# Optimization experiments

Measured on AMD Instinct MI355X. Metric: run time of the kernel, lower is better.

The kernel has to match this reference:

```python
import jax, jax.numpy as jnp
import numpy as np

N = 80000
E = 1280000
EPS = 1e-5

def _lrelu(x):
    return jax.nn.leaky_relu(x, 0.01)

def _bn(h):
    # training-mode BatchNorm1d with batch size 1: stats over the node dim; affine is identity at init
    return (h - h.mean(0)) / jnp.sqrt(h.var(0) + EPS)

def _ln(h, g, b):
    m = h.mean(-1, keepdims=True)
    v = h.var(-1, keepdims=True)
    return (h - m) / jnp.sqrt(v + EPS) * g + b

def _gcn(h, w, b, src, dst, n):
    # PyG GCNConv: add self loops, symmetric deg^-1/2 normalization, aggregate at target
    hw = h @ w.T
    loop = jnp.arange(n, dtype=src.dtype)
    s = jnp.concatenate([src, loop])
    d = jnp.concatenate([dst, loop])
    deg = jax.ops.segment_sum(jnp.ones(d.shape, hw.dtype), d, num_segments=n)
    dinv = jnp.where(deg > 0, 1.0 / jnp.sqrt(deg), 0.0)
    msg = hw[s] * (dinv[s] * dinv[d])[:, None]  # [E+N, C]
    return jax.ops.segment_sum(msg, d, num_segments=n) + b

def _tnet(x, c1w, c1b, c2w, c2b, c3w, c3b, f1w, f1b, f2w, f2b, f3w, f3b):
    h = jax.nn.relu(x @ c1w.T + c1b)          # [N,64]  (source skips bn1)
    h = jax.nn.relu(_bn(h @ c2w.T + c2b))     # [N,128]
    h = jax.nn.relu(_bn(h @ c3w.T + c3b))     # [N,1024]
    g = h.max(0)                              # global max pool -> [1024]
    g = jax.nn.relu(g @ f1w.T + f1b)
    g = jax.nn.relu(g @ f2w.T + f2b)
    iden = jnp.array([1.0, 0.0, 0.0, 0.0, 1.0, 0.0, 0.0, 0.0, 1.0], x.dtype)
    g = g @ f3w.T + f3b + iden
    return g.reshape(3, 3)

def _forward(edge_index, x, tnet_c1_w, tnet_c1_b, tnet_c2_w, tnet_c2_b, tnet_c3_w, tnet_c3_b, tnet_fc1_w, tnet_fc1_b, tnet_fc2_w, tnet_fc2_b, tnet_fc3_w, tnet_fc3_b, conv1_w, conv1_b, g1_li_w, g1_li_b, g1_gcn_w, g1_gcn_b, g1_ln_g, g1_ln_b, conv2_w, conv2_b, g2_li_w, g2_li_b, g2_gcn_w, g2_gcn_b, g2_ln_g, g2_ln_b, conv3_w, conv3_b, out_w, out_b):
    src, dst = edge_index[0], edge_index[1]
    n = x.shape[0]
    T = _tnet(x, tnet_c1_w, tnet_c1_b, tnet_c2_w, tnet_c2_b, tnet_c3_w, tnet_c3_b, tnet_fc1_w, tnet_fc1_b, tnet_fc2_w, tnet_fc2_b, tnet_fc3_w, tnet_fc3_b)
    h0 = x @ T                                  # [N,3] spatial transform
    xg = _lrelu(h0 @ conv1_w.T + conv1_b)       # [N,64] (conv1d k=1 == per-node linear)
    # Gcn_Attention 1
    nf = _lrelu(xg @ g1_li_w.T + g1_li_b)
    nf2 = _lrelu(_gcn(nf, g1_gcn_w, g1_gcn_b, src, dst, n))
    h = _ln(jnp.concatenate([nf, nf2], 1), g1_ln_g, g1_ln_b)   # [N,128]
    h = _lrelu(h @ conv2_w.T + conv2_b)
    # Gcn_Attention 2
    nf = _lrelu(h @ g2_li_w.T + g2_li_b)
    nf2 = _lrelu(_gcn(nf, g2_gcn_w, g2_gcn_b, src, dst, n))
    h = _ln(jnp.concatenate([nf, nf2], 1), g2_ln_g, g2_ln_b)   # [N,256]
    h = jnp.concatenate([h, xg], 1)                            # [N,320]
    h = _lrelu(h @ conv3_w.T + conv3_b)                        # [N,256]
    pooled = h.mean(0)                                         # global mean pool (single graph)
    feat = jnp.concatenate([jnp.broadcast_to(pooled, (n, pooled.shape[0])), xg], 1)  # [N,320]
    return feat @ out_w.T + out_b                              # [N,4]

def setup_inputs():
    ki = iter(jax.random.split(jax.random.key(0), 32))
    def W(shape):
        return jax.random.normal(next(ki), shape, jnp.float32) * (1.0 / float(np.sqrt(shape[-1])))
    z = lambda n: jnp.zeros((n,), jnp.float32)
    o = lambda n: jnp.ones((n,), jnp.float32)
    inp = {}
    inp['x'] = jax.random.normal(next(ki), (N, 3), jnp.float32)
    inp['edge_index'] = jax.random.randint(next(ki), (2, E), 0, N, dtype=jnp.int32)
    inp['tnet_c1_w'] = W((64, 3)); inp['tnet_c1_b'] = z(64)
    inp['tnet_c2_w'] = W((128, 64)); inp['tnet_c2_b'] = z(128)
    inp['tnet_c3_w'] = W((1024, 128)); inp['tnet_c3_b'] = z(1024)
    inp['tnet_fc1_w'] = W((512, 1024)); inp['tnet_fc1_b'] = z(512)
    inp['tnet_fc2_w'] = W((256, 512)); inp['tnet_fc2_b'] = z(256)
    inp['tnet_fc3_w'] = W((9, 256)); inp['tnet_fc3_b'] = z(9)
    inp['conv1_w'] = W((64, 3)); inp['conv1_b'] = z(64)
    inp['g1_li_w'] = W((64, 64)); inp['g1_li_b'] = z(64)
    inp['g1_gcn_w'] = W((64, 64)); inp['g1_gcn_b'] = z(64)
    inp['g1_ln_g'] = o(128); inp['g1_ln_b'] = z(128)
    inp['conv2_w'] = W((128, 128)); inp['conv2_b'] = z(128)
    inp['g2_li_w'] = W((128, 128)); inp['g2_li_b'] = z(128)
    inp['g2_gcn_w'] = W((128, 128)); inp['g2_gcn_b'] = z(128)
    inp['g2_ln_g'] = o(256); inp['g2_ln_b'] = z(256)
    inp['conv3_w'] = W((256, 320)); inp['conv3_b'] = z(256)
    inp['out_w'] = W((4, 320)); inp['out_b'] = z(4)
    return inp

def reference(x, edge_index, tnet_c1_w, tnet_c1_b, tnet_c2_w, tnet_c2_b, tnet_c3_w, tnet_c3_b, tnet_fc1_w, tnet_fc1_b, tnet_fc2_w, tnet_fc2_b, tnet_fc3_w, tnet_fc3_b, conv1_w, conv1_b, g1_li_w, g1_li_b, g1_gcn_w, g1_gcn_b, g1_ln_g, g1_ln_b, conv2_w, conv2_b, g2_li_w, g2_li_b, g2_gcn_w, g2_gcn_b, g2_ln_g, g2_ln_b, conv3_w, conv3_b, out_w, out_b):
    return _forward(edge_index, x, tnet_c1_w, tnet_c1_b, tnet_c2_w, tnet_c2_b, tnet_c3_w, tnet_c3_b, tnet_fc1_w, tnet_fc1_b, tnet_fc2_w, tnet_fc2_b, tnet_fc3_w, tnet_fc3_b, conv1_w, conv1_b, g1_li_w, g1_li_b, g1_gcn_w, g1_gcn_b, g1_ln_g, g1_ln_b, conv2_w, conv2_b, g2_li_w, g2_li_b, g2_gcn_w, g2_gcn_b, g2_ln_g, g2_ln_b, conv3_w, conv3_b, out_w, out_b)
```

## Files before the change

kernel.cpp:

```cpp
#include <hip/hip_runtime.h>
#include <cstddef>

#define EPSV 1e-5f

typedef __attribute__((ext_vector_type(8))) short frag8;
typedef __attribute__((ext_vector_type(4))) float f32x4;

__device__ __forceinline__ float lrelu01(float v) { return v > 0.f ? v : 0.01f * v; }
__device__ __forceinline__ void atomAddF(float* p, float v) { unsafeAtomicAdd(p, v); }
__device__ __forceinline__ unsigned fkey(float f) {
    unsigned u = __float_as_uint(f);
    return (u & 0x80000000u) ? ~u : (u | 0x80000000u);
}
__device__ __forceinline__ unsigned short f2b(float f) {
    unsigned u = __float_as_uint(f);
    unsigned r = u + 0x7fffu + ((u >> 16) & 1u);
    return (unsigned short)(r >> 16);
}
__device__ __forceinline__ float b2f(unsigned short h) {
    return __uint_as_float(((unsigned)h) << 16);
}
__device__ __forceinline__ float blo(unsigned u) { return __uint_as_float(u << 16); }
__device__ __forceinline__ float bhi(unsigned u) { return __uint_as_float(u & 0xffff0000u); }

static inline unsigned cdivu(unsigned a, unsigned b) { return (a + b - 1) / b; }


__device__ void degrank_body(int bid, const int* __restrict__ dst, int* __restrict__ deg,
                             int* __restrict__ rank, int E) {
    int e = bid * 256 + threadIdx.x;
    if (e < E) rank[e] = atomicAdd(&deg[dst[e]], 1);
}

__device__ void scan_local_body(int bid, const int* __restrict__ deg, int* __restrict__ startv,
                                int* __restrict__ bsum, float* __restrict__ dinv, int n) {
    __shared__ int t0[256];
    int tid = threadIdx.x;
    int i = bid * 256 + tid;
    int v = (i < n) ? deg[i] : 0;
    if (i < n) dinv[i] = rsqrtf((float)(v + 1));
    t0[tid] = v;
    __syncthreads();
    for (int o = 1; o < 256; o <<= 1) {
        int add = (tid >= o) ? t0[tid - o] : 0;
        __syncthreads();
        t0[tid] += add;
        __syncthreads();
    }
    if (i < n) startv[i] = t0[tid] - v;
    if (tid == 255) bsum[bid] = t0[255];
}

__device__ void scan_bsum_body(int* __restrict__ bsum, int nb) {
    __shared__ int t0[512];
    __shared__ int t1[512];
    int tid = threadIdx.x;
    int v0 = (tid < nb) ? bsum[tid] : 0;
    int v1 = (tid + 256 < nb) ? bsum[tid + 256] : 0;
    t0[tid] = v0; t0[tid + 256] = v1;
    __syncthreads();
    int* a = t0; int* b = t1;
    for (int o = 1; o < 512; o <<= 1) {
        b[tid]       = a[tid]       + ((tid >= o)       ? a[tid - o]       : 0);
        b[tid + 256] = a[tid + 256] + ((tid + 256 >= o) ? a[tid + 256 - o] : 0);
        __syncthreads();
        int* t = a; a = b; b = t;
    }
    if (tid < nb) bsum[tid] = a[tid] - v0;
    if (tid + 256 < nb) bsum[tid + 256] = a[tid + 256] - v1;
}

__device__ void scan_add_body(int bid, int* __restrict__ startv, const int* __restrict__ bsum, int n) {
    int i = bid * 256 + threadIdx.x;
    if (i < n) startv[i] += bsum[bid];
}

__device__ void fill_body(int bid, const int* __restrict__ src, const int* __restrict__ dst,
                          const int* __restrict__ rank, const int* __restrict__ startv,
                          int* __restrict__ csr, int E) {
    int e = bid * 256 + threadIdx.x;
    if (e < E) csr[startv[dst[e]] + rank[e]] = src[e];
}


__device__ void wconv_body(int bid, const float* __restrict__ s0, const float* __restrict__ s1,
                           const float* __restrict__ s2, const float* __restrict__ s3,
                           const float* __restrict__ s4, const float* __restrict__ s5,
                           const float* __restrict__ s6, const float* __restrict__ s7,
                           unsigned short* __restrict__ dst) {
    int t = bid * 256 + threadIdx.x;
    if (t >= 278528) return;
    const float* srcs[8] = {s0, s1, s2, s3, s4, s5, s6, s7};
    const int off[9] = {0, 8192, 139264, 143360, 147456, 163840, 180224, 196608, 278528};
    int seg = 0;
    while (t >= off[seg + 1]) ++seg;
    unsigned short v = f2b(srcs[seg][t - off[seg]]);
    if (seg == 1) {
        int li = t - 8192;
        int rch = li >> 7, k = li & 127;
        int cb = rch >> 7, r = rch & 127;
        int flat = ((r >> 4) * 4 + (k >> 5)) * 64 + ((k >> 3) & 3) * 16 + (r & 15);
        dst[8192 + cb * 16384 + flat * 8 + (k & 7)] = v;
    } else {
        dst[t] = v;
    }
}

__device__ void h1_body(int bid, const float* __restrict__ x, const float* __restrict__ w,
                        const float* __restrict__ b, unsigned short* __restrict__ h1, int n) {
    int node = bid * 256 + threadIdx.x;
    if (node >= n) return;
    float x0 = x[node * 3], x1 = x[node * 3 + 1], x2 = x[node * 3 + 2];
    unsigned short* o = h1 + (size_t)node * 64;
#pragma unroll
    for (int cp = 0; cp < 8; ++cp) {
        unsigned short tmp[8];
#pragma unroll
        for (int t = 0; t < 8; ++t) {
            int c = cp * 8 + t;
            float v = x0 * w[c * 3] + x1 * w[c * 3 + 1] + x2 * w[c * 3 + 2] + b[c];
            tmp[t] = f2b(fmaxf(v, 0.f));
        }
        *(float4*)(o + cp * 8) = *(float4*)tmp;
    }
}

__device__ void prebn_body(int bid, const float* __restrict__ z, const float* __restrict__ sum2,
                           const float* __restrict__ ss2, unsigned short* __restrict__ a3f,
                           int n16, float invn) {
    int t = bid * 256 + threadIdx.x;
    if (t >= n16) return;
    int row = t >> 4, cp = t & 15;
    int c = cp * 8;
    const float* src = z + (size_t)row * 128 + c;
    float4 v0 = *(const float4*)src;
    float4 v1 = *(const float4*)(src + 4);
    float vv[8] = {v0.x, v0.y, v0.z, v0.w, v1.x, v1.y, v1.z, v1.w};
    unsigned short o[8];
#pragma unroll
    for (int i = 0; i < 8; ++i) {
        float m = sum2[c + i] * invn;
        float var = ss2[c + i] * invn - m * m;
        o[i] = f2b(fmaxf((vv[i] - m) * rsqrtf(var + EPSV), 0.f));
    }
    int tile = row >> 7, r = row & 127;
    int flat = ((r >> 4) * 4 + (cp >> 2)) * 64 + (cp & 3) * 16 + (r & 15);
    *(float4*)(a3f + (size_t)tile * 16384 + flat * 8) = *(float4*)o;
}

__device__ void fc1_body(int bid, const float* __restrict__ sum3, const float* __restrict__ ss3,
                         const unsigned* __restrict__ maxk,
                         const float* __restrict__ f1w, const float* __restrict__ f1b,
                         float* __restrict__ a1, float invn) {
    __shared__ float g[1024];
    int tid = threadIdx.x;
    for (int c = tid; c < 1024; c += 256) {
        float m = sum3[c] * invn;
        float var = ss3[c] * invn - m * m;
        unsigned k = maxk[c];
        unsigned u = (k & 0x80000000u) ? (k & 0x7FFFFFFFu) : ~k;
        g[c] = fmaxf((__uint_as_float(u) - m) * rsqrtf(var + EPSV), 0.f);
    }
    __syncthreads();
    int row = bid * 64 + (tid >> 2);
    int part = tid & 3;
    const float* w = f1w + (size_t)row * 1024 + part * 256;
    const float* gg = g + part * 256;
    float s = 0.f;
#pragma unroll 4
    for (int k = 0; k < 256; k += 4) {
        float4 wv = *(const float4*)(w + k);
        s = fmaf(wv.x, gg[k], s);
        s = fmaf(wv.y, gg[k + 1], s);
        s = fmaf(wv.z, gg[k + 2], s);
        s = fmaf(wv.w, gg[k + 3], s);
    }
    s += __shfl_xor(s, 1); s += __shfl_xor(s, 2);
    if (part == 0) a1[row] = fmaxf(s + f1b[row], 0.f);
}

enum { MF_BIAS = 1, MF_LRELU = 2, MF_DINV = 4, MF_STOREF = 8, MF_STOREB = 16,
       MF_STATS = 32, MF_COLSUM = 64 };

template <int BN, int MODE>
__device__ void mgemm_body(int bx, int by,
                           const unsigned short* __restrict__ A, int lda, int K,
                           const unsigned short* __restrict__ W,
                           const float* __restrict__ bias,
                           float* __restrict__ OutF, unsigned short* __restrict__ OutB, int ldo,
                           const float* __restrict__ dinv,
                           float* __restrict__ sum_o, float* __restrict__ ss_o,
                           unsigned* __restrict__ maxk_o) {
    constexpr int BM = 128;
    constexpr int LDT = 40;
    __shared__ unsigned short As[BM * LDT];
    __shared__ unsigned short Ws[BN * LDT];
    __shared__ float redS[2 * 128];
    __shared__ unsigned redM[128];

    const int tid = threadIdx.x;
    const int wid = tid >> 6, lane = tid & 63;
    const int quad = lane >> 4, lrow = lane & 15;
    const int bn0 = bx * BM;
    const int bc0 = by * BN;

    constexpr int NI = (BN == 128) ? 4 : 2;
    constexpr int NJ = 4;
    const int wm = (BN == 128) ? (wid & 1) * 64 : wid * 32;
    const int wn = (BN == 128) ? (wid >> 1) * 64 : 0;

    if (MODE & (MF_STATS | MF_COLSUM)) {
        for (int c = tid; c < BN; c += 256) {
            redS[c] = 0.f; redS[128 + c] = 0.f; redM[c] = 0u;
        }
    }

    f32x4 acc[NI][NJ] = {};

    for (int k0 = 0; k0 < K; k0 += 32) {
#pragma unroll
        for (int h = 0; h < 2; ++h) {
            int ch = tid + h * 256;
            int row = ch >> 2, cp = ch & 3;
            const unsigned short* src = A + (size_t)(bn0 + row) * lda + k0 + cp * 8;
            *(float4*)&As[row * LDT + cp * 8] = *(const float4*)src;
        }
#pragma unroll
        for (int h = 0; h < BN / 64; ++h) {
            int ch = tid + h * 256;
            int row = ch >> 2, cp = ch & 3;
            const unsigned short* src = W + (size_t)(bc0 + row) * K + k0 + cp * 8;
            *(float4*)&Ws[row * LDT + cp * 8] = *(const float4*)src;
        }
        __syncthreads();
        frag8 af[NI], bf[NJ];
#pragma unroll
        for (int i = 0; i < NI; ++i)
            af[i] = *(const frag8*)&As[(wm + i * 16 + lrow) * LDT + quad * 8];
#pragma unroll
        for (int j = 0; j < NJ; ++j)
            bf[j] = *(const frag8*)&Ws[(wn + j * 16 + lrow) * LDT + quad * 8];
#pragma unroll
        for (int i = 0; i < NI; ++i)
#pragma unroll
            for (int j = 0; j < NJ; ++j)
                acc[i][j] = __builtin_amdgcn_mfma_f32_16x16x32_bf16(af[i], bf[j], acc[i][j], 0, 0, 0);
        __syncthreads();
    }

#pragma unroll
    for (int j = 0; j < NJ; ++j) {
        const int col = bc0 + wn + j * 16 + lrow;
        float bv = (MODE & MF_BIAS) ? bias[col] : 0.f;
        float s = 0.f, q = 0.f, m = -3.4e38f;
#pragma unroll
        for (int i = 0; i < NI; ++i) {
            const int rowb = bn0 + wm + i * 16 + quad * 4;
#pragma unroll
            for (int r = 0; r < 4; ++r) {
                float t = acc[i][j][r] + bv;
                if (MODE & MF_LRELU) t = lrelu01(t);
                if (MODE & MF_DINV) t *= dinv[rowb + r];
                if (MODE & MF_STOREF) OutF[(size_t)(rowb + r) * ldo + col] = t;
                if (MODE & MF_STOREB) OutB[(size_t)(rowb + r) * ldo + col] = f2b(t);
                s += t; q += t * t; m = fmaxf(m, t);
            }
        }
        if (MODE & (MF_STATS | MF_COLSUM)) {
            s += __shfl_xor(s, 16); s += __shfl_xor(s, 32);
            if (MODE & MF_STATS) {
                q += __shfl_xor(q, 16); q += __shfl_xor(q, 32);
                m = fmaxf(m, __shfl_xor(m, 16)); m = fmaxf(m, __shfl_xor(m, 32));
            }
            if (quad == 0) {
                int lc = wn + j * 16 + lrow;
                atomicAdd(&redS[lc], s);
                if (MODE & MF_STATS) {
                    atomicAdd(&redS[128 + lc], q);
                    atomicMax(&redM[lc], fkey(m));
                }
            }
        }
    }
    if (MODE & (MF_STATS | MF_COLSUM)) {
        __syncthreads();
        for (int c = tid; c < BN; c += 256) {
            atomAddF(&sum_o[bc0 + c], redS[c]);
            if (MODE & MF_STATS) {
                atomAddF(&ss_o[bc0 + c], redS[128 + c]);
                atomicMax(&maxk_o[bc0 + c], redM[c]);
            }
        }
    }
}

template <int BN, int MODE, int SWAP>
__launch_bounds__(256)
__global__ void k_mgemm(const unsigned short* __restrict__ A, int lda, int K,
                        const unsigned short* __restrict__ W,
                        const float* __restrict__ bias,
                        float* __restrict__ OutF, unsigned short* __restrict__ OutB, int ldo,
                        const float* __restrict__ dinv,
                        float* __restrict__ sum_o, float* __restrict__ ss_o,
                        unsigned* __restrict__ maxk_o) {
    int bx = SWAP ? blockIdx.y : blockIdx.x;
    int by = SWAP ? blockIdx.x : blockIdx.y;
    mgemm_body<BN, MODE>(bx, by, A, lda, K, W, bias, OutF, OutB, ldo, dinv, sum_o, ss_o, maxk_o);
}

__device__ void z3_body(int bid,
                        const unsigned short* __restrict__ AF,
                        const unsigned short* __restrict__ WF,
                        const float* __restrict__ bias,
                        float* __restrict__ sum_o, float* __restrict__ ss_o,
                        unsigned* __restrict__ maxk_o, int ntiles) {
    const int tid = threadIdx.x;
    const int wid = tid >> 6, lane = tid & 63;
    const int quad = lane >> 4, lrow = lane & 15;

    int w = (bid & 7) * ntiles + (bid >> 3);
    const int tile = w >> 3;
    const int cb = w & 7;
    const unsigned short* At = AF + (size_t)tile * 16384;
    const unsigned short* Wt = WF + (size_t)cb * 16384;

    const int ar = (wid & 1) * 4;
    const int wc = (wid >> 1) * 4;
    f32x4 acc[4][4] = {};
#pragma unroll
    for (int kc = 0; kc < 4; ++kc) {
        frag8 af[4], bf[4];
#pragma unroll
        for (int i = 0; i < 4; ++i)
            af[i] = *(const frag8*)&At[(((ar + i) * 4 + kc) * 64 + lane) * 8];
#pragma unroll
        for (int j = 0; j < 4; ++j)
            bf[j] = *(const frag8*)&Wt[(((wc + j) * 4 + kc) * 64 + lane) * 8];
#pragma unroll
        for (int i = 0; i < 4; ++i)
#pragma unroll
            for (int j = 0; j < 4; ++j)
                acc[i][j] = __builtin_amdgcn_mfma_f32_16x16x32_bf16(af[i], bf[j], acc[i][j], 0, 0, 0);
    }

#pragma unroll
    for (int j = 0; j < 4; ++j) {
        int c = cb * 128 + (wc + j) * 16 + lrow;
        float bv = bias[c];
        float s = 0.f, q = 0.f, m = -3.4e38f;
#pragma unroll
        for (int i = 0; i < 4; ++i)
#pragma unroll
            for (int r = 0; r < 4; ++r) {
                float t = acc[i][j][r] + bv;
                s += t; q += t * t; m = fmaxf(m, t);
            }
        s += __shfl_xor(s, 16); s += __shfl_xor(s, 32);
        q += __shfl_xor(q, 16); q += __shfl_xor(q, 32);
        m = fmaxf(m, __shfl_xor(m, 16)); m = fmaxf(m, __shfl_xor(m, 32));
        if (quad == 0) {
            atomAddF(&sum_o[c], s);
            atomAddF(&ss_o[c], q);
            atomicMax(&maxk_o[c], fkey(m));
        }
    }
}


__launch_bounds__(256)
__global__ void FK1(const int* __restrict__ dst, int* __restrict__ deg, int* __restrict__ rank,
                    int E, int EB,
                    const float* s0, const float* s1, const float* s2, const float* s3,
                    const float* s4, const float* s5, const float* s6, const float* s7,
                    unsigned short* __restrict__ WB, int WCB,
                    const float* __restrict__ x, const float* __restrict__ c1w,
                    const float* __restrict__ c1b, unsigned short* __restrict__ B1, int n) {
    int b = blockIdx.x;
    if (b < EB) { degrank_body(b, dst, deg, rank, E); return; }
    b -= EB;
    if (b < WCB) { wconv_body(b, s0, s1, s2, s3, s4, s5, s6, s7, WB); return; }
    b -= WCB;
    h1_body(b, x, c1w, c1b, B1, n);
}

__launch_bounds__(256)
__global__ void FK2(const unsigned short* __restrict__ A, int lda, int K,
                    const unsigned short* __restrict__ W, const float* __restrict__ bias,
                    float* __restrict__ OutF, int ldo,
                    float* __restrict__ sum_o, float* __restrict__ ss_o,
                    unsigned* __restrict__ maxk_o, int GXz,
                    const int* __restrict__ deg, int* __restrict__ startv,
                    int* __restrict__ bsum, float* __restrict__ dinvv, int n) {
    if ((int)blockIdx.x < GXz)
        mgemm_body<128, (MF_BIAS | MF_STOREF | MF_STATS)>(
            blockIdx.x, 0, A, lda, K, W, bias, OutF, nullptr, ldo, nullptr, sum_o, ss_o, maxk_o);
    else
        scan_local_body(blockIdx.x - GXz, deg, startv, bsum, dinvv, n);
}

__launch_bounds__(256)
__global__ void FK3(const float* __restrict__ z, const float* __restrict__ sum2,
                    const float* __restrict__ ss2, unsigned short* __restrict__ a3f,
                    int n16, float invn, int PB, int* __restrict__ bsum, int nb) {
    if ((int)blockIdx.x < PB) prebn_body(blockIdx.x, z, sum2, ss2, a3f, n16, invn);
    else scan_bsum_body(bsum, nb);
}

__launch_bounds__(256)
__global__ void FK4(const unsigned short* __restrict__ AF, const unsigned short* __restrict__ WF,
                    const float* __restrict__ bias,
                    float* __restrict__ sum_o, float* __restrict__ ss_o,
                    unsigned* __restrict__ maxk_o, int ntiles, int NZ,
                    int* __restrict__ startv, const int* __restrict__ bsum, int n) {
    if ((int)blockIdx.x < NZ) z3_body(blockIdx.x, AF, WF, bias, sum_o, ss_o, maxk_o, ntiles);
    else scan_add_body(blockIdx.x - NZ, startv, bsum, n);
}

__launch_bounds__(256)
__global__ void FK5(const int* __restrict__ src, const int* __restrict__ dst,
                    const int* __restrict__ rank, const int* __restrict__ startv,
                    int* __restrict__ csr, int E,
                    const float* __restrict__ sum3, const float* __restrict__ ss3,
                    const unsigned* __restrict__ maxk,
                    const float* __restrict__ f1w, const float* __restrict__ f1b,
                    float* __restrict__ a1, float invn) {
    int b = blockIdx.x;
    if (b < 8) { fc1_body(b, sum3, ss3, maxk, f1w, f1b, a1, invn); return; }
    fill_body(b - 8, src, dst, rank, startv, csr, E);
}

__launch_bounds__(256)
__global__ void k_fc2(const float* __restrict__ a1, const float* __restrict__ f2w,
                      const float* __restrict__ f2bias, float* __restrict__ a2) {
    __shared__ float a1s[512];
    int tid = threadIdx.x;
    a1s[tid] = a1[tid];
    a1s[tid + 256] = a1[tid + 256];
    __syncthreads();
    int row = blockIdx.x * 32 + (tid >> 3);
    int part = tid & 7;
    const float* w = f2w + (size_t)row * 512 + part * 64;
    const float* aa = a1s + part * 64;
    float s = 0.f;
#pragma unroll 4
    for (int k = 0; k < 64; k += 4) {
        float4 wv = *(const float4*)(w + k);
        s = fmaf(wv.x, aa[k], s);
        s = fmaf(wv.y, aa[k + 1], s);
        s = fmaf(wv.z, aa[k + 2], s);
        s = fmaf(wv.w, aa[k + 3], s);
    }
    s += __shfl_xor(s, 1); s += __shfl_xor(s, 2); s += __shfl_xor(s, 4);
    if (part == 0) a2[row] = fmaxf(s + f2bias[row], 0.f);
}

template <int CH>
__launch_bounds__(256)
__global__ void k_gln(const int* __restrict__ startv, const int* __restrict__ degv,
                      const int* __restrict__ csr, const unsigned short* __restrict__ q,
                      const unsigned short* __restrict__ nf, const float* __restrict__ dinv,
                      const float* __restrict__ gcn_b, const float* __restrict__ lng,
                      const float* __restrict__ lnb, unsigned short* __restrict__ outp,
                      int ldo, int n) {
    constexpr int GRP = (CH == 64) ? 8 : 4;
    constexpr int PL  = 64 / GRP;
    constexpr int TT  = 16 / GRP;
    constexpr int CPL = CH / PL;
    const int wv = threadIdx.x >> 6, lane = threadIdx.x & 63;
    const int g = lane / PL, p = lane & (PL - 1);
    int node = blockIdx.x * 4 + wv;
    if (node >= n) return;

    const unsigned short* qp = q + (size_t)p * CPL;

    float acc[CPL];
    {
        uint4 v = *(const uint4*)(qp + (size_t)node * CH);
        unsigned sv[4] = {v.x, v.y, v.z, v.w};
        if (g == 0) {
#pragma unroll
            for (int d = 0; d < 4; ++d) { acc[2 * d] = blo(sv[d]); acc[2 * d + 1] = bhi(sv[d]); }
        } else {
#pragma unroll
            for (int k = 0; k < CPL; ++k) acc[k] = 0.f;
        }
    }

    int s0 = startv[node], cnt = degv[node];
    const int* cs = csr + s0;
    int sidx[TT];
#pragma unroll
    for (int t = 0; t < TT; ++t) { int j = t * GRP + g; sidx[t] = (j < cnt) ? cs[j] : n; }
    for (int j0 = 0; j0 < cnt; j0 += 16) {
        uint4 buf[TT];
#pragma unroll
        for (int t = 0; t < TT; ++t)
            buf[t] = *(const uint4*)(qp + (size_t)(unsigned)sidx[t] * CH);
#pragma unroll
        for (int t = 0; t < TT; ++t) {
            int j = j0 + 16 + t * GRP + g;
            sidx[t] = (j < cnt) ? cs[j] : n;
        }
#pragma unroll
        for (int t = 0; t < TT; ++t) {
            unsigned bw[4] = {buf[t].x, buf[t].y, buf[t].z, buf[t].w};
#pragma unroll
            for (int d = 0; d < 4; ++d) {
                acc[2 * d] += blo(bw[d]);
                acc[2 * d + 1] += bhi(bw[d]);
            }
        }
    }

#pragma unroll
    for (int k = 0; k < CPL; ++k) {
#pragma unroll
        for (int off = PL; off < 64; off <<= 1) acc[k] += __shfl_xor(acc[k], off);
    }

    float di = dinv[node];
    float nv[CPL], bv[CPL];
    {
        uint4 v = *(const uint4*)(nf + (size_t)node * CH + p * CPL);
        unsigned sv[4] = {v.x, v.y, v.z, v.w};
#pragma unroll
        for (int d = 0; d < 4; ++d) { nv[2 * d] = blo(sv[d]); nv[2 * d + 1] = bhi(sv[d]); }
    }
    const float* gb = gcn_b + p * CPL;
#pragma unroll
    for (int k = 0; k < CPL; ++k) bv[k] = lrelu01(di * acc[k] + gb[k]);

    float s = 0.f, ss = 0.f;
#pragma unroll
    for (int k = 0; k < CPL; ++k) { s += nv[k] + bv[k]; ss += nv[k] * nv[k] + bv[k] * bv[k]; }
#pragma unroll
    for (int off = 32; off > 0; off >>= 1) { s += __shfl_xor(s, off); ss += __shfl_xor(ss, off); }
    const float inv = 1.f / (float)(GRP * 2 * CH);
    float mu = s * inv;
    float var = ss * inv - mu * mu;
    float rsg = rsqrtf(var + EPSV);

    unsigned short* orow = outp + (size_t)node * ldo;
    if (g == 0) {
        unsigned short tmp[CPL];
        const float* lg = lng + p * CPL; const float* lb = lnb + p * CPL;
#pragma unroll
        for (int k = 0; k < CPL; ++k) tmp[k] = f2b((nv[k] - mu) * rsg * lg[k] + lb[k]);
        *(uint4*)(orow + p * CPL) = *(uint4*)tmp;
    } else if (g == 1) {
        unsigned short tmp[CPL];
        const float* lg = lng + CH + p * CPL; const float* lb = lnb + CH + p * CPL;
#pragma unroll
        for (int k = 0; k < CPL; ++k) tmp[k] = f2b((bv[k] - mu) * rsg * lg[k] + lb[k]);
        *(uint4*)(orow + CH + p * CPL) = *(uint4*)tmp;
    }
}


__launch_bounds__(256)
__global__ void k_xg2(const float* __restrict__ x, const float* __restrict__ a2,
                      const float* __restrict__ f3w, const float* __restrict__ f3b,
                      const float* __restrict__ w, const float* __restrict__ b,
                      unsigned short* __restrict__ xg, int n) {
    __shared__ float a2s[256];
    __shared__ float T9s[9];
    int tid = threadIdx.x;
    a2s[tid] = a2[tid];
    __syncthreads();
    if (tid < 144) {
        int r = tid >> 4, kk = (tid & 15) * 16;
        const float* wr = f3w + r * 256 + kk;
        const float* ar = a2s + kk;
        float s = 0.f;
#pragma unroll
        for (int k = 0; k < 16; ++k) s = fmaf(wr[k], ar[k], s);
        s += __shfl_xor(s, 1); s += __shfl_xor(s, 2);
        s += __shfl_xor(s, 4); s += __shfl_xor(s, 8);
        if ((tid & 15) == 0) {
            s += f3b[r];
            if (r == 0 || r == 4 || r == 8) s += 1.f;
            T9s[r] = s;
        }
    }
    __syncthreads();
    int node = blockIdx.x * 256 + tid;
    if (node >= n) return;
    float x0 = x[node * 3], x1 = x[node * 3 + 1], x2 = x[node * 3 + 2];
    float h0 = x0 * T9s[0] + x1 * T9s[3] + x2 * T9s[6];
    float h1 = x0 * T9s[1] + x1 * T9s[4] + x2 * T9s[7];
    float h2 = x0 * T9s[2] + x1 * T9s[5] + x2 * T9s[8];
    unsigned short* o = xg + (size_t)node * 320;
#pragma unroll
    for (int cp = 0; cp < 8; ++cp) {
        unsigned short tmp[8];
#pragma unroll
        for (int t = 0; t < 8; ++t) {
            int c = cp * 8 + t;
            float v = h0 * w[c * 3] + h1 * w[c * 3 + 1] + h2 * w[c * 3 + 2] + b[c];
            tmp[t] = f2b(lrelu01(v));
        }
        *(float4*)(o + cp * 8) = *(float4*)tmp;
    }
}

template <int BN>
__launch_bounds__(256)
__global__ void k_ligc(const unsigned short* __restrict__ A, int lda, int K,
                       const unsigned short* __restrict__ Wli, const float* __restrict__ bli,
                       const unsigned short* __restrict__ Wgc, const float* __restrict__ dinv,
                       unsigned short* __restrict__ NF, int ldnf,
                       unsigned short* __restrict__ Q, int ldq) {
    constexpr int BM = 128;
    constexpr int LDT = 40;
    constexpr int LDT2 = BN + 8;
    __shared__ unsigned short SA[BM * LDT2];
    __shared__ unsigned short Ws[BN * LDT];

    const int tid = threadIdx.x;
    const int wid = tid >> 6, lane = tid & 63;
    const int quad = lane >> 4, lrow = lane & 15;
    const int bn0 = blockIdx.x * BM;
    constexpr int NI = (BN == 128) ? 4 : 2;
    constexpr int NJ = 4;
    const int wm = (BN == 128) ? (wid & 1) * 64 : wid * 32;
    const int wn = (BN == 128) ? (wid >> 1) * 64 : 0;

    {
        f32x4 acc[NI][NJ] = {};
        for (int k0 = 0; k0 < K; k0 += 32) {
#pragma unroll
            for (int h = 0; h < 2; ++h) {
                int ch = tid + h * 256;
                int row = ch >> 2, cp = ch & 3;
                *(float4*)&SA[row * LDT + cp * 8] =
                    *(const float4*)(A + (size_t)(bn0 + row) * lda + k0 + cp * 8);
            }
#pragma unroll
            for (int h = 0; h < BN / 64; ++h) {
                int ch = tid + h * 256;
                int row = ch >> 2, cp = ch & 3;
                *(float4*)&Ws[row * LDT + cp * 8] =
                    *(const float4*)(Wli + (size_t)row * K + k0 + cp * 8);
            }
            __syncthreads();
            frag8 af[NI], bf[NJ];
#pragma unroll
            for (int i = 0; i < NI; ++i)
                af[i] = *(const frag8*)&SA[(wm + i * 16 + lrow) * LDT + quad * 8];
#pragma unroll
            for (int j = 0; j < NJ; ++j)
                bf[j] = *(const frag8*)&Ws[(wn + j * 16 + lrow) * LDT + quad * 8];
#pragma unroll
            for (int i = 0; i < NI; ++i)
#pragma unroll
                for (int j = 0; j < NJ; ++j)
                    acc[i][j] = __builtin_amdgcn_mfma_f32_16x16x32_bf16(af[i], bf[j], acc[i][j], 0, 0, 0);
            __syncthreads();
        }
#pragma unroll
        for (int j = 0; j < NJ; ++j) {
            const int col = wn + j * 16 + lrow;
            float bv = bli[col];
#pragma unroll
            for (int i = 0; i < NI; ++i) {
                const int rowl = wm + i * 16 + quad * 4;
#pragma unroll
                for (int r = 0; r < 4; ++r) {
                    unsigned short h = f2b(lrelu01(acc[i][j][r] + bv));
                    NF[(size_t)(bn0 + rowl + r) * ldnf + col] = h;
                    SA[(rowl + r) * LDT2 + col] = h;
                }
            }
        }
        __syncthreads();
    }
    {
        f32x4 acc[NI][NJ] = {};
        for (int k0 = 0; k0 < BN; k0 += 32) {
#pragma unroll
            for (int h = 0; h < BN / 64; ++h) {
                int ch = tid + h * 256;
                int row = ch >> 2, cp = ch & 3;
                *(float4*)&Ws[row * LDT + cp * 8] =
                    *(const float4*)(Wgc + (size_t)row * BN + k0 + cp * 8);
            }
            __syncthreads();
            frag8 af[NI], bf[NJ];
#pragma unroll
            for (int i = 0; i < NI; ++i)
                af[i] = *(const frag8*)&SA[(wm + i * 16 + lrow) * LDT2 + k0 + quad * 8];
#pragma unroll
            for (int j = 0; j < NJ; ++j)
                bf[j] = *(const frag8*)&Ws[(wn + j * 16 + lrow) * LDT + quad * 8];
#pragma unroll
            for (int i = 0; i < NI; ++i)
#pragma unroll
                for (int j = 0; j < NJ; ++j)
                    acc[i][j] = __builtin_amdgcn_mfma_f32_16x16x32_bf16(af[i], bf[j], acc[i][j], 0, 0, 0);
            __syncthreads();
        }
#pragma unroll
        for (int j = 0; j < NJ; ++j) {
            const int col = wn + j * 16 + lrow;
#pragma unroll
            for (int i = 0; i < NI; ++i) {
                const int rowb = bn0 + wm + i * 16 + quad * 4;
#pragma unroll
                for (int r = 0; r < 4; ++r) {
                    float t = acc[i][j][r] * dinv[rowb + r];
                    Q[(size_t)(rowb + r) * ldq + col] = f2b(t);
                }
            }
        }
    }
}

__global__ void k_out2(const unsigned short* __restrict__ hcat, const float* __restrict__ ow,
                       const float* __restrict__ ob, const float* __restrict__ pooled,
                       float* __restrict__ out, int n, float invn) {
    __shared__ float c4s[4];
    int tid = threadIdx.x;
    {
        int j = tid >> 6, lane = tid & 63;
        float s = 0.f;
        for (int c = lane; c < 256; c += 64) s += pooled[c] * invn * ow[j * 320 + c];
#pragma unroll
        for (int off = 32; off > 0; off >>= 1) s += __shfl_down(s, off);
        if (lane == 0) c4s[j] = s + ob[j];
    }
    __syncthreads();
    int node = blockIdx.x * 256 + tid;
    if (node >= n) return;
    const unsigned short* xgp = hcat + (size_t)node * 320 + 256;
    float s0 = c4s[0], s1 = c4s[1], s2 = c4s[2], s3 = c4s[3];
#pragma unroll
    for (int cp = 0; cp < 8; ++cp) {
        float4 raw = *(const float4*)(xgp + cp * 8);
        unsigned short tmp[8];
        *(float4*)tmp = raw;
#pragma unroll
        for (int t = 0; t < 8; ++t) {
            int k = 256 + cp * 8 + t;
            float f = b2f(tmp[t]);
            s0 = fmaf(f, ow[k], s0);
            s1 = fmaf(f, ow[320 + k], s1);
            s2 = fmaf(f, ow[640 + k], s2);
            s3 = fmaf(f, ow[960 + k], s3);
        }
    }
    *(float4*)(out + (size_t)node * 4) = make_float4(s0, s1, s2, s3);
}


extern "C" void kernel_launch(void* const* d_in, const int* in_sizes, int n_in,
                              void* d_out, int out_size, void* d_ws, size_t ws_size,
                              hipStream_t stream) {
    const float* x   = (const float*)d_in[0];
    const int*   ei  = (const int*)d_in[1];
    const float* c1w = (const float*)d_in[2];  const float* c1b = (const float*)d_in[3];
    const float* c2w = (const float*)d_in[4];  const float* c2b = (const float*)d_in[5];
    const float* c3w = (const float*)d_in[6];  const float* c3b = (const float*)d_in[7];
    const float* f1w = (const float*)d_in[8];  const float* f1b = (const float*)d_in[9];
    const float* f2w = (const float*)d_in[10]; const float* f2bp = (const float*)d_in[11];
    const float* f3w = (const float*)d_in[12]; const float* f3b = (const float*)d_in[13];
    const float* cv1w = (const float*)d_in[14]; const float* cv1b = (const float*)d_in[15];
    const float* li1w = (const float*)d_in[16]; const float* li1b = (const float*)d_in[17];
    const float* gc1w = (const float*)d_in[18]; const float* gc1b = (const float*)d_in[19];
    const float* ln1g = (const float*)d_in[20]; const float* ln1b = (const float*)d_in[21];
    const float* cv2w = (const float*)d_in[22]; const float* cv2b = (const float*)d_in[23];
    const float* li2w = (const float*)d_in[24]; const float* li2b = (const float*)d_in[25];
    const float* gc2w = (const float*)d_in[26]; const float* gc2b = (const float*)d_in[27];
    const float* ln2g = (const float*)d_in[28]; const float* ln2b = (const float*)d_in[29];
    const float* cv3w = (const float*)d_in[30]; const float* cv3b = (const float*)d_in[31];
    const float* ow  = (const float*)d_in[32]; const float* ob  = (const float*)d_in[33];
    float* out = (float*)d_out;

    const int N = in_sizes[0] / 3;
    const int E = in_sizes[1] / 2;
    const int* srcI = ei;
    const int* dstI = ei + E;

    char* base = (char*)d_ws;
    size_t off = 0;
    auto take = [&](size_t bytes) -> char* {
        char* p = base + off;
        off = (off + bytes + 255) & ~(size_t)255;
        return p;
    };
    int*   deg    = (int*)  take((size_t)N * 4);
    float* dinv   = (float*)take((size_t)N * 4);
    int*   startv = (int*)  take((size_t)N * 4);
    int*   rank   = (int*)  take((size_t)E * 4);
    int*   csr    = (int*)  take((size_t)E * 4);
    int*   bsum   = (int*)  take(512 * 4);
    float* sm     = (float*)take(8192 * 4);
    unsigned short* WB = (unsigned short*)take(278528 * 2);
    unsigned short* H  = (unsigned short*)take((size_t)N * 320 * 2);
    float* F1 = (float*)take((size_t)N * 128 * 4);
    unsigned short* B1 = (unsigned short*)take((size_t)N * 64 * 2);
    unsigned short* B2 = (unsigned short*)take(((size_t)N * 128 + 128) * 2);
    unsigned short* B3 = (unsigned short*)take((size_t)N * 128 * 2);

    unsigned short* c2wb  = WB + 0;
    unsigned short* c3wf  = WB + 8192;
    unsigned short* li1wb = WB + 139264;
    unsigned short* gc1wb = WB + 143360;
    unsigned short* cv2wb = WB + 147456;
    unsigned short* li2wb = WB + 163840;
    unsigned short* gc2wb = WB + 180224;
    unsigned short* cv3wb = WB + 196608;

    float* sum2 = sm + 0;    float* ss2 = sm + 128;
    float* sum3 = sm + 256;  float* ss3 = sm + 1280;
    unsigned* maxk = (unsigned*)(sm + 2304);
    float* pooled = sm + 3328;
    unsigned* dmax = (unsigned*)(sm + 3584);
    float* a1  = sm + 5120;
    float* a2  = sm + 5760;

    const float invn = 1.0f / (float)N;
    const dim3 blk(256);
    const unsigned GX = (unsigned)(N / 128);
    const unsigned NB = cdivu((unsigned)N, 256);
    const unsigned EB = cdivu((unsigned)E, 256);
    const unsigned WCB = cdivu(278528u, 256);
    const unsigned PB = cdivu((unsigned)N * 16, 256);

    hipMemsetAsync(deg, 0, (size_t)N * 4, stream);
    hipMemsetAsync(sm, 0, 3712 * 4, stream);
    hipMemsetAsync(B2 + (size_t)N * 128, 0, 256, stream);

    FK1<<<EB + WCB + NB, blk, 0, stream>>>(dstI, deg, rank, E, (int)EB,
                                           c2w, c3w, li1w, gc1w, cv2w, li2w, gc2w, cv3w,
                                           WB, (int)WCB, x, c1w, c1b, B1, N);
    FK2<<<GX + NB, blk, 0, stream>>>(B1, 64, 64, c2wb, c2b, F1, 128,
                                     sum2, ss2, dmax, (int)GX, deg, startv, bsum, dinv, N);
    FK3<<<PB + 1, blk, 0, stream>>>(F1, sum2, ss2, B2, N * 16, invn, (int)PB, bsum, (int)NB);
    FK4<<<8 * GX + NB, blk, 0, stream>>>(B2, c3wf, c3b, sum3, ss3, maxk, (int)GX,
                                         (int)(8 * GX), startv, bsum, N);
    hipMemsetAsync(B2 + (size_t)N * 64, 0, 128, stream);
    FK5<<<8 + EB, blk, 0, stream>>>(srcI, dstI, rank, startv, csr, E,
                                    sum3, ss3, maxk, f1w, f1b, a1, invn);
    k_fc2<<<8, blk, 0, stream>>>(a1, f2w, f2bp, a2);
    k_xg2<<<NB, blk, 0, stream>>>(x, a2, f3w, f3b, cv1w, cv1b, H + 256, N);

    k_ligc<64><<<GX, blk, 0, stream>>>(H + 256, 320, 64, li1wb, li1b, gc1wb, dinv, B1, 64, B2, 64);
    k_gln<64><<<cdivu((unsigned)N, 4), blk, 0, stream>>>(
        startv, deg, csr, B2, B1, dinv, gc1b, ln1g, ln1b, B3, 128, N);
    k_mgemm<128, (MF_BIAS | MF_LRELU | MF_STOREB), 0><<<dim3(GX, 1), blk, 0, stream>>>(
        B3, 128, 128, cv2wb, cv2b, nullptr, B2, 128, nullptr, nullptr, nullptr, nullptr);

    k_ligc<128><<<GX, blk, 0, stream>>>(B2, 128, 128, li2wb, li2b, gc2wb, dinv, B3, 128, B2, 128);
    k_gln<128><<<cdivu((unsigned)N, 4), blk, 0, stream>>>(
        startv, deg, csr, B2, B3, dinv, gc2b, ln2g, ln2b, H, 320, N);

    k_mgemm<128, (MF_BIAS | MF_LRELU | MF_COLSUM), 1><<<dim3(2, GX), blk, 0, stream>>>(
        H, 320, 320, cv3wb, cv3b, nullptr, nullptr, 0, nullptr, pooled, nullptr, nullptr);

    k_out2<<<NB, blk, 0, stream>>>(H, ow, ob, pooled, out, N, invn);
}
```

Baseline: 506.7 us.

## Fold scan-add into CSR fill, fuse T-net FC layers, precompute xg output dot

Drops the separate scan-add pass by adding the block offset (bsum) on the fly in the CSR fill and in the GCN aggregation. The fill then moves into FK4 alongside the conv3 GEMM. The three T-net FC layers are fused into one 8-block kernel with atomic-counter grid barriers, removing two launches. The xg part of the output projection is now computed in k_xg2 and written as a 4-float per-node buffer, so k_out2 no longer re-reads the bf16 xg columns. The costs are a spin barrier that relies on all 8 blocks being co-resident, and an extra per-node buffer.

```diff
diff --git a/kernel.cpp b/kernel.cpp
--- a/kernel.cpp
+++ b/kernel.cpp
@@ -24,6 +24,17 @@
 __device__ __forceinline__ float bhi(unsigned u) { return __uint_as_float(u & 0xffff0000u); }
 
 static inline unsigned cdivu(unsigned a, unsigned b) { return (a + b - 1) / b; }
+
+__device__ __forceinline__ void gbar(unsigned* cnt, unsigned target) {
+    __syncthreads();
+    if (threadIdx.x == 0) {
+        __threadfence();
+        atomicAdd(cnt, 1u);
+        while (atomicAdd(cnt, 0u) < target) { }
+        __threadfence();
+    }
+    __syncthreads();
+}
 
 
 __device__ void degrank_body(int bid, const int* __restrict__ dst, int* __restrict__ deg,
@@ -70,16 +81,14 @@
     if (tid + 256 < nb) bsum[tid + 256] = a[tid + 256] - v1;
 }
 
-__device__ void scan_add_body(int bid, int* __restrict__ startv, const int* __restrict__ bsum, int n) {
-    int i = bid * 256 + threadIdx.x;
-    if (i < n) startv[i] += bsum[bid];
-}
-
 __device__ void fill_body(int bid, const int* __restrict__ src, const int* __restrict__ dst,
                           const int* __restrict__ rank, const int* __restrict__ startv,
-                          int* __restrict__ csr, int E) {
+                          const int* __restrict__ bsum, int* __restrict__ csr, int E) {
     int e = bid * 256 + threadIdx.x;
-    if (e < E) csr[startv[dst[e]] + rank[e]] = src[e];
+    if (e < E) {
+        int d = dst[e];
+        csr[startv[d] + bsum[d >> 8] + rank[e]] = src[e];
+    }
 }
 
 
@@ -148,37 +157,6 @@
     *(float4*)(a3f + (size_t)tile * 16384 + flat * 8) = *(float4*)o;
 }
 
-__device__ void fc1_body(int bid, const float* __restrict__ sum3, const float* __restrict__ ss3,
-                         const unsigned* __restrict__ maxk,
-                         const float* __restrict__ f1w, const float* __restrict__ f1b,
-                         float* __restrict__ a1, float invn) {
-    __shared__ float g[1024];
-    int tid = threadIdx.x;
-    for (int c = tid; c < 1024; c += 256) {
-        float m = sum3[c] * invn;
-        float var = ss3[c] * invn - m * m;
-        unsigned k = maxk[c];
-        unsigned u = (k & 0x80000000u) ? (k & 0x7FFFFFFFu) : ~k;
-        g[c] = fmaxf((__uint_as_float(u) - m) * rsqrtf(var + EPSV), 0.f);
-    }
-    __syncthreads();
-    int row = bid * 64 + (tid >> 2);
-    int part = tid & 3;
-    const float* w = f1w + (size_t)row * 1024 + part * 256;
-    const float* gg = g + part * 256;
-    float s = 0.f;
-#pragma unroll 4
-    for (int k = 0; k < 256; k += 4) {
-        float4 wv = *(const float4*)(w + k);
-        s = fmaf(wv.x, gg[k], s);
-        s = fmaf(wv.y, gg[k + 1], s);
-        s = fmaf(wv.z, gg[k + 2], s);
-        s = fmaf(wv.w, gg[k + 3], s);
-    }
-    s += __shfl_xor(s, 1); s += __shfl_xor(s, 2);
-    if (part == 0) a1[row] = fmaxf(s + f1b[row], 0.f);
-}
-
 enum { MF_BIAS = 1, MF_LRELU = 2, MF_DINV = 4, MF_STOREF = 8, MF_STOREB = 16,
        MF_STATS = 32, MF_COLSUM = 64 };
 
@@ -411,52 +389,93 @@
                     const float* __restrict__ bias,
                     float* __restrict__ sum_o, float* __restrict__ ss_o,
                     unsigned* __restrict__ maxk_o, int ntiles, int NZ,
-                    int* __restrict__ startv, const int* __restrict__ bsum, int n) {
+                    const int* __restrict__ src, const int* __restrict__ dst,
+                    const int* __restrict__ rank, const int* __restrict__ startv,
+                    const int* __restrict__ bsum, int* __restrict__ csr, int E) {
     if ((int)blockIdx.x < NZ) z3_body(blockIdx.x, AF, WF, bias, sum_o, ss_o, maxk_o, ntiles);
-    else scan_add_body(blockIdx.x - NZ, startv, bsum, n);
+    else fill_body(blockIdx.x - NZ, src, dst, rank, startv, bsum, csr, E);
 }
 
 __launch_bounds__(256)
-__global__ void FK5(const int* __restrict__ src, const int* __restrict__ dst,
-                    const int* __restrict__ rank, const int* __restrict__ startv,
-                    int* __restrict__ csr, int E,
-                    const float* __restrict__ sum3, const float* __restrict__ ss3,
-                    const unsigned* __restrict__ maxk,
-                    const float* __restrict__ f1w, const float* __restrict__ f1b,
-                    float* __restrict__ a1, float invn) {
-    int b = blockIdx.x;
-    if (b < 8) { fc1_body(b, sum3, ss3, maxk, f1w, f1b, a1, invn); return; }
-    fill_body(b - 8, src, dst, rank, startv, csr, E);
-}
-
-__launch_bounds__(256)
-__global__ void k_fc2(const float* __restrict__ a1, const float* __restrict__ f2w,
-                      const float* __restrict__ f2bias, float* __restrict__ a2) {
+__global__ void k_tnet(const float* __restrict__ sum3, const float* __restrict__ ss3,
+                       const unsigned* __restrict__ maxk,
+                       const float* __restrict__ f1w, const float* __restrict__ f1b,
+                       const float* __restrict__ f2w, const float* __restrict__ f2bias,
+                       const float* __restrict__ f3w, const float* __restrict__ f3b,
+                       float* __restrict__ a1, float* __restrict__ a2,
+                       float* __restrict__ T9,
+                       unsigned* __restrict__ cnt1, unsigned* __restrict__ cnt2, float invn) {
+    __shared__ float g[1024];
     __shared__ float a1s[512];
     int tid = threadIdx.x;
+    int bid = blockIdx.x;
+    for (int c = tid; c < 1024; c += 256) {
+        float m = sum3[c] * invn;
+        float var = ss3[c] * invn - m * m;
+        unsigned k = maxk[c];
+        unsigned u = (k & 0x80000000u) ? (k & 0x7FFFFFFFu) : ~k;
+        g[c] = fmaxf((__uint_as_float(u) - m) * rsqrtf(var + EPSV), 0.f);
+    }
+    __syncthreads();
+    {
+        int row = bid * 64 + (tid >> 2);
+        int part = tid & 3;
+        const float* w = f1w + (size_t)row * 1024 + part * 256;
+        const float* gg = g + part * 256;
+        float s = 0.f;
+#pragma unroll 4
+        for (int k = 0; k < 256; k += 4) {
+            float4 wv = *(const float4*)(w + k);
+            s = fmaf(wv.x, gg[k], s);
+            s = fmaf(wv.y, gg[k + 1], s);
+            s = fmaf(wv.z, gg[k + 2], s);
+            s = fmaf(wv.w, gg[k + 3], s);
+        }
+        s += __shfl_xor(s, 1); s += __shfl_xor(s, 2);
+        if (part == 0) a1[row] = fmaxf(s + f1b[row], 0.f);
+    }
+    gbar(cnt1, 8);
     a1s[tid] = a1[tid];
     a1s[tid + 256] = a1[tid + 256];
     __syncthreads();
-    int row = blockIdx.x * 32 + (tid >> 3);
-    int part = tid & 7;
-    const float* w = f2w + (size_t)row * 512 + part * 64;
-    const float* aa = a1s + part * 64;
-    float s = 0.f;
+    {
+        int row = bid * 32 + (tid >> 3);
+        int part = tid & 7;
+        const float* w = f2w + (size_t)row * 512 + part * 64;
+        const float* aa = a1s + part * 64;
+        float s = 0.f;
 #pragma unroll 4
-    for (int k = 0; k < 64; k += 4) {
-        float4 wv = *(const float4*)(w + k);
-        s = fmaf(wv.x, aa[k], s);
-        s = fmaf(wv.y, aa[k + 1], s);
-        s = fmaf(wv.z, aa[k + 2], s);
-        s = fmaf(wv.w, aa[k + 3], s);
-    }
-    s += __shfl_xor(s, 1); s += __shfl_xor(s, 2); s += __shfl_xor(s, 4);
-    if (part == 0) a2[row] = fmaxf(s + f2bias[row], 0.f);
+        for (int k = 0; k < 64; k += 4) {
+            float4 wv = *(const float4*)(w + k);
+            s = fmaf(wv.x, aa[k], s);
+            s = fmaf(wv.y, aa[k + 1], s);
+            s = fmaf(wv.z, aa[k + 2], s);
+            s = fmaf(wv.w, aa[k + 3], s);
+        }
+        s += __shfl_xor(s, 1); s += __shfl_xor(s, 2); s += __shfl_xor(s, 4);
+        if (part == 0) a2[row] = fmaxf(s + f2bias[row], 0.f);
+    }
+    gbar(cnt2, 8);
+    if (bid == 0 && tid < 144) {
+        int r = tid >> 4, kk = (tid & 15) * 16;
+        const float* wr = f3w + r * 256 + kk;
+        float s = 0.f;
+#pragma unroll
+        for (int k = 0; k < 16; ++k) s = fmaf(wr[k], a2[kk + k], s);
+        s += __shfl_xor(s, 1); s += __shfl_xor(s, 2);
+        s += __shfl_xor(s, 4); s += __shfl_xor(s, 8);
+        if ((tid & 15) == 0) {
+            s += f3b[r];
+            if (r == 0 || r == 4 || r == 8) s += 1.f;
+            T9[r] = s;
+        }
+    }
 }
 
 template <int CH>
 __launch_bounds__(256)
-__global__ void k_gln(const int* __restrict__ startv, const int* __restrict__ degv,
+__global__ void k_gln(const int* __restrict__ startv, const int* __restrict__ bsum,
+                      const int* __restrict__ degv,
                       const int* __restrict__ csr, const unsigned short* __restrict__ q,
                       const unsigned short* __restrict__ nf, const float* __restrict__ dinv,
                       const float* __restrict__ gcn_b, const float* __restrict__ lng,
@@ -486,7 +505,7 @@
         }
     }
 
-    int s0 = startv[node], cnt = degv[node];
+    int s0 = startv[node] + bsum[node >> 8], cnt = degv[node];
     const int* cs = csr + s0;
     int sidx[TT];
 #pragma unroll
@@ -558,30 +577,15 @@
 
 
 __launch_bounds__(256)
-__global__ void k_xg2(const float* __restrict__ x, const float* __restrict__ a2,
-                      const float* __restrict__ f3w, const float* __restrict__ f3b,
+__global__ void k_xg2(const float* __restrict__ x, const float* __restrict__ T9,
                       const float* __restrict__ w, const float* __restrict__ b,
-                      unsigned short* __restrict__ xg, int n) {
-    __shared__ float a2s[256];
+                      const float* __restrict__ ow,
+                      unsigned short* __restrict__ xg, float* __restrict__ xdot, int n) {
+    __shared__ float owS[256];
     __shared__ float T9s[9];
     int tid = threadIdx.x;
-    a2s[tid] = a2[tid];
-    __syncthreads();
-    if (tid < 144) {
-        int r = tid >> 4, kk = (tid & 15) * 16;
-        const float* wr = f3w + r * 256 + kk;
-        const float* ar = a2s + kk;
-        float s = 0.f;
-#pragma unroll
-        for (int k = 0; k < 16; ++k) s = fmaf(wr[k], ar[k], s);
-        s += __shfl_xor(s, 1); s += __shfl_xor(s, 2);
-        s += __shfl_xor(s, 4); s += __shfl_xor(s, 8);
-        if ((tid & 15) == 0) {
-            s += f3b[r];
-            if (r == 0 || r == 4 || r == 8) s += 1.f;
-            T9s[r] = s;
-        }
-    }
+    owS[tid] = ow[(tid >> 6) * 320 + 256 + (tid & 63)];
+    if (tid < 9) T9s[tid] = T9[tid];
     __syncthreads();
     int node = blockIdx.x * 256 + tid;
     if (node >= n) return;
@@ -590,17 +594,23 @@
     float h1 = x0 * T9s[1] + x1 * T9s[4] + x2 * T9s[7];
     float h2 = x0 * T9s[2] + x1 * T9s[5] + x2 * T9s[8];
     unsigned short* o = xg + (size_t)node * 320;
+    float d0 = 0.f, d1 = 0.f, d2 = 0.f, d3 = 0.f;
 #pragma unroll
     for (int cp = 0; cp < 8; ++cp) {
         unsigned short tmp[8];
 #pragma unroll
         for (int t = 0; t < 8; ++t) {
             int c = cp * 8 + t;
-            float v = h0 * w[c * 3] + h1 * w[c * 3 + 1] + h2 * w[c * 3 + 2] + b[c];
-            tmp[t] = f2b(lrelu01(v));
+            float v = lrelu01(h0 * w[c * 3] + h1 * w[c * 3 + 1] + h2 * w[c * 3 + 2] + b[c]);
+            tmp[t] = f2b(v);
+            d0 = fmaf(v, owS[c], d0);
+            d1 = fmaf(v, owS[64 + c], d1);
+            d2 = fmaf(v, owS[128 + c], d2);
+            d3 = fmaf(v, owS[192 + c], d3);
         }
         *(float4*)(o + cp * 8) = *(float4*)tmp;
     }
+    *(float4*)(xdot + (size_t)node * 4) = make_float4(d0, d1, d2, d3);
 }
 
 template <int BN>
@@ -715,7 +725,7 @@
     }
 }
 
-__global__ void k_out2(const unsigned short* __restrict__ hcat, const float* __restrict__ ow,
+__global__ void k_out2(const float* __restrict__ xdot, const float* __restrict__ ow,
                        const float* __restrict__ ob, const float* __restrict__ pooled,
                        float* __restrict__ out, int n, float invn) {
     __shared__ float c4s[4];
@@ -731,24 +741,9 @@
     __syncthreads();
     int node = blockIdx.x * 256 + tid;
     if (node >= n) return;
-    const unsigned short* xgp = hcat + (size_t)node * 320 + 256;
-    float s0 = c4s[0], s1 = c4s[1], s2 = c4s[2], s3 = c4s[3];
-#pragma unroll
-    for (int cp = 0; cp < 8; ++cp) {
-        float4 raw = *(const float4*)(xgp + cp * 8);
-        unsigned short tmp[8];
-        *(float4*)tmp = raw;
-#pragma unroll
-        for (int t = 0; t < 8; ++t) {
-            int k = 256 + cp * 8 + t;
-            float f = b2f(tmp[t]);
-            s0 = fmaf(f, ow[k], s0);
-            s1 = fmaf(f, ow[320 + k], s1);
-            s2 = fmaf(f, ow[640 + k], s2);
-            s3 = fmaf(f, ow[960 + k], s3);
-        }
-    }
-    *(float4*)(out + (size_t)node * 4) = make_float4(s0, s1, s2, s3);
+    float4 xd = *(const float4*)(xdot + (size_t)node * 4);
+    *(float4*)(out + (size_t)node * 4) =
+        make_float4(c4s[0] + xd.x, c4s[1] + xd.y, c4s[2] + xd.z, c4s[3] + xd.w);
 }
 
 
@@ -800,6 +795,7 @@
     unsigned short* B1 = (unsigned short*)take((size_t)N * 64 * 2);
     unsigned short* B2 = (unsigned short*)take(((size_t)N * 128 + 128) * 2);
     unsigned short* B3 = (unsigned short*)take((size_t)N * 128 * 2);
+    float* XD = (float*)take((size_t)N * 4 * 4);
 
     unsigned short* c2wb  = WB + 0;
     unsigned short* c3wf  = WB + 8192;
@@ -815,6 +811,9 @@
     unsigned* maxk = (unsigned*)(sm + 2304);
     float* pooled = sm + 3328;
     unsigned* dmax = (unsigned*)(sm + 3584);
+    unsigned* cnt1 = (unsigned*)(sm + 3712);
+    unsigned* cnt2 = (unsigned*)(sm + 3713);
+    float* T9  = sm + 3968;
     float* a1  = sm + 5120;
     float* a2  = sm + 5760;
 
@@ -827,7 +826,7 @@
     const unsigned PB = cdivu((unsigned)N * 16, 256);
 
     hipMemsetAsync(deg, 0, (size_t)N * 4, stream);
-    hipMemsetAsync(sm, 0, 3712 * 4, stream);
+    hipMemsetAsync(sm, 0, 3720 * 4, stream);
     hipMemsetAsync(B2 + (size_t)N * 128, 0, 256, stream);
 
     FK1<<<EB + WCB + NB, blk, 0, stream>>>(dstI, deg, rank, E, (int)EB,
@@ -836,26 +835,25 @@
     FK2<<<GX + NB, blk, 0, stream>>>(B1, 64, 64, c2wb, c2b, F1, 128,
                                      sum2, ss2, dmax, (int)GX, deg, startv, bsum, dinv, N);
     FK3<<<PB + 1, blk, 0, stream>>>(F1, sum2, ss2, B2, N * 16, invn, (int)PB, bsum, (int)NB);
-    FK4<<<8 * GX + NB, blk, 0, stream>>>(B2, c3wf, c3b, sum3, ss3, maxk, (int)GX,
-                                         (int)(8 * GX), startv, bsum, N);
+    FK4<<<8 * GX + EB, blk, 0, stream>>>(B2, c3wf, c3b, sum3, ss3, maxk, (int)GX,
+                                         (int)(8 * GX), srcI, dstI, rank, startv, bsum, csr, E);
     hipMemsetAsync(B2 + (size_t)N * 64, 0, 128, stream);
-    FK5<<<8 + EB, blk, 0, stream>>>(srcI, dstI, rank, startv, csr, E,
-                                    sum3, ss3, maxk, f1w, f1b, a1, invn);
-    k_fc2<<<8, blk, 0, stream>>>(a1, f2w, f2bp, a2);
-    k_xg2<<<NB, blk, 0, stream>>>(x, a2, f3w, f3b, cv1w, cv1b, H + 256, N);
+    k_tnet<<<8, blk, 0, stream>>>(sum3, ss3, maxk, f1w, f1b, f2w, f2bp, f3w, f3b,
+                                  a1, a2, T9, cnt1, cnt2, invn);
+    k_xg2<<<NB, blk, 0, stream>>>(x, T9, cv1w, cv1b, ow, H + 256, XD, N);
 
     k_ligc<64><<<GX, blk, 0, stream>>>(H + 256, 320, 64, li1wb, li1b, gc1wb, dinv, B1, 64, B2, 64);
     k_gln<64><<<cdivu((unsigned)N, 4), blk, 0, stream>>>(
-        startv, deg, csr, B2, B1, dinv, gc1b, ln1g, ln1b, B3, 128, N);
+        startv, bsum, deg, csr, B2, B1, dinv, gc1b, ln1g, ln1b, B3, 128, N);
     k_mgemm<128, (MF_BIAS | MF_LRELU | MF_STOREB), 0><<<dim3(GX, 1), blk, 0, stream>>>(
         B3, 128, 128, cv2wb, cv2b, nullptr, B2, 128, nullptr, nullptr, nullptr, nullptr);
 
     k_ligc<128><<<GX, blk, 0, stream>>>(B2, 128, 128, li2wb, li2b, gc2wb, dinv, B3, 128, B2, 128);
     k_gln<128><<<cdivu((unsigned)N, 4), blk, 0, stream>>>(
-        startv, deg, csr, B2, B3, dinv, gc2b, ln2g, ln2b, H, 320, N);
+        startv, bsum, deg, csr, B2, B3, dinv, gc2b, ln2g, ln2b, H, 320, N);
 
     k_mgemm<128, (MF_BIAS | MF_LRELU | MF_COLSUM), 1><<<dim3(2, GX), blk, 0, stream>>>(
         H, 320, 320, cv3wb, cv3b, nullptr, nullptr, 0, nullptr, pooled, nullptr, nullptr);
 
-    k_out2<<<NB, blk, 0, stream>>>(H, ow, ob, pooled, out, N, invn);
-}
+    k_out2<<<NB, blk, 0, stream>>>(XD, ow, ob, pooled, out, N, invn);
+}
```

After: 504.4 us. No clear change (-0.5%).
